# Kernel optimization log

Measured on AMD Instinct MI355X. Metric: run time of the kernel, lower is better.

The kernel has to match this reference:

```python
import jax, jax.numpy as jnp
import numpy as np

B, S, E, H, L, V = 4, 1024, 256, 512, 16, 8000


def setup_inputs() -> dict:
    key = jax.random.key(0)
    ks = jax.random.split(key, 8)
    return {
        "sent": jax.random.randint(ks[0], (B, S), 0, V),
        "mask": jax.random.randint(ks[1], (B, S), 0, 2),
        "char_emb_w": jax.random.normal(ks[2], (V, E), dtype=jnp.float32) * 0.02,
        "mask_emb_w": jax.random.normal(ks[3], (2, E), dtype=jnp.float32) * 0.02,
        "wA": jax.random.normal(ks[4], (E, H), dtype=jnp.float32) * (1.0 / np.sqrt(E)),
        "bA": jnp.zeros((H,), dtype=jnp.float32),
        "wB": jax.random.normal(ks[5], (E, H), dtype=jnp.float32) * (1.0 / np.sqrt(E)),
        "bB": jnp.zeros((H,), dtype=jnp.float32),
        "wS": jax.random.normal(ks[6], (E, L), dtype=jnp.float32) * (1.0 / np.sqrt(E)),
        "bS": jnp.zeros((L,), dtype=jnp.float32),
    }


def reference(sent, mask, char_emb_w, mask_emb_w, wA, bA, wB, bB, wS, bS):
    # Embedding lookups: (B,S,E)
    ce = char_emb_w[sent]
    me = mask_emb_w[mask]
    # vemb = char_emb * GELU(mask_emb)  (torch GELU default = exact erf form)
    vemb = ce * jax.nn.gelu(me, approximate=False)
    va = vemb @ wA + bA                      # (B,S,H)
    vb = jax.nn.sigmoid(vemb @ wB + bB)      # (B,S,H)
    vc = jnp.einsum("bih,bjh->bij", va, vb) / H   # (B,S,S), biaffine score
    vd = jax.nn.relu(vemb @ wS + bS)         # (B,S,L)
    # torch: matmul(vc.unsqueeze(3), vd.unsqueeze(2)) -> (B,S,S,L) rank-1 outer product
    pred = jax.nn.softmax(vc[..., None] * vd[:, :, None, :], axis=-1)
    return pred
```

## Files before the change

### kernel.cpp

```cpp
#include <hip/hip_runtime.h>
#include <hip/hip_bf16.h>
#include <math.h>

typedef __attribute__((ext_vector_type(8))) short short8;
typedef __attribute__((ext_vector_type(4))) float f32x4;
typedef unsigned short u16;

#define Bn 4
#define Sn 1024
#define En 256
#define Hn 512
#define Ln 16

__device__ inline u16 bf16b(float x) {
    union { __hip_bfloat16 h; u16 u; } cvt;
    cvt.h = __float2bfloat16(x);
    return cvt.u;
}

__global__ void prep_wt(const float* __restrict__ wA, const float* __restrict__ wB,
                        const float* __restrict__ wS, u16* __restrict__ Wt) {
    int idx = blockIdx.x * 256 + threadIdx.x;
    int n = idx >> 8;
    int k = idx & 255;
    float v = 0.f;
    if (n < 512)       v = wA[k * 512 + n];
    else if (n < 1024) v = wB[k * 512 + (n - 512)];
    else if (n < 1040) v = wS[k * 16 + (n - 1024)];
    Wt[idx] = bf16b(v);
}

__global__ void embed_gelu(const int* __restrict__ sent, const int* __restrict__ mask,
                           const float* __restrict__ ce_w, const float* __restrict__ me_w,
                           u16* __restrict__ vemb) {
    int row = blockIdx.x;
    int e = threadIdx.x;
    int s = sent[row];
    int m = mask[row];
    float ce = ce_w[s * En + e];
    float me = me_w[m * En + e];
    float g = 0.5f * me * (1.f + erff(me * 0.70710678118654752f));
    vemb[row * En + e] = bf16b(ce * g);
}

#define LDP 136
__global__ __launch_bounds__(256, 2) void gemm1(const u16* __restrict__ A, const u16* __restrict__ Bt,
                                                const float* __restrict__ bA, const float* __restrict__ bB,
                                                const float* __restrict__ bS,
                                                u16* __restrict__ va, u16* __restrict__ vb,
                                                float* __restrict__ vd) {
    __shared__ __align__(16) u16 As[64 * LDP];
    __shared__ __align__(16) u16 Bs[64 * LDP];
    int tid = threadIdx.x;
    int m0 = blockIdx.x * 64, n0 = blockIdx.y * 64;
    int lane = tid & 63, w = tid >> 6;
    int lrow = lane & 15, quad = lane >> 4;

    f32x4 acc[4];
    for (int nt = 0; nt < 4; nt++) acc[nt] = (f32x4){0.f, 0.f, 0.f, 0.f};

    for (int kb = 0; kb < 2; kb++) {
        for (int i = 0; i < 4; i++) {
            int off = (i * 256 + tid) * 8;
            int r = off >> 7, c = off & 127;
            *(short8*)&As[r * LDP + c] = *(const short8*)&A[(m0 + r) * 256 + kb * 128 + c];
            *(short8*)&Bs[r * LDP + c] = *(const short8*)&Bt[(n0 + r) * 256 + kb * 128 + c];
        }
        __syncthreads();
        for (int ks = 0; ks < 4; ks++) {
            short8 a = *(const short8*)&As[(w * 16 + lrow) * LDP + ks * 32 + quad * 8];
            for (int nt = 0; nt < 4; nt++) {
                short8 b = *(const short8*)&Bs[(nt * 16 + lrow) * LDP + ks * 32 + quad * 8];
                acc[nt] = __builtin_amdgcn_mfma_f32_16x16x32_bf16(a, b, acc[nt], 0, 0, 0);
            }
        }
        __syncthreads();
    }
    int mbase = m0 + w * 16 + quad * 4;
    for (int nt = 0; nt < 4; nt++) {
        int n = n0 + nt * 16 + lrow;
        for (int r = 0; r < 4; r++) {
            float v = acc[nt][r];
            int mm = mbase + r;
            if (n < 512) {
                va[mm * 512 + n] = bf16b(v + bA[n]);
            } else if (n < 1024) {
                float x = v + bB[n - 512];
                vb[mm * 512 + (n - 512)] = bf16b(1.f / (1.f + __expf(-x)));
            } else if (n < 1040) {
                float x = v + bS[n - 1024];
                vd[mm * 16 + (n - 1024)] = x > 0.f ? x : 0.f;
            }
        }
    }
}

__global__ void dminmax(const float* __restrict__ vd, float* __restrict__ dmn, float* __restrict__ dmx) {
    int r = blockIdx.x * 256 + threadIdx.x;
    float mn = 1e30f, mx = -1e30f;
    for (int l = 0; l < 16; l++) {
        float v = vd[r * 16 + l];
        mn = fminf(mn, v);
        mx = fmaxf(mx, v);
    }
    dmn[r] = mn;
    dmx[r] = mx;
}

__global__ __launch_bounds__(256, 2) void gemm2(const u16* __restrict__ va_g, const u16* __restrict__ vb_g,
                                                float* __restrict__ vc) {
    __shared__ __align__(16) u16 As[64 * LDP];
    __shared__ __align__(16) u16 Bs[64 * LDP];
    int tid = threadIdx.x;
    int b = blockIdx.z;
    int m0 = blockIdx.x * 64, n0 = blockIdx.y * 64;
    const u16* A  = va_g + (size_t)b * 1024 * 512;
    const u16* Bt = vb_g + (size_t)b * 1024 * 512;
    int lane = tid & 63, w = tid >> 6;
    int lrow = lane & 15, quad = lane >> 4;

    f32x4 acc[4];
    for (int nt = 0; nt < 4; nt++) acc[nt] = (f32x4){0.f, 0.f, 0.f, 0.f};

    for (int kb = 0; kb < 4; kb++) {
        for (int i = 0; i < 4; i++) {
            int off = (i * 256 + tid) * 8;
            int r = off >> 7, c = off & 127;
            *(short8*)&As[r * LDP + c] = *(const short8*)&A[(m0 + r) * 512 + kb * 128 + c];
            *(short8*)&Bs[r * LDP + c] = *(const short8*)&Bt[(n0 + r) * 512 + kb * 128 + c];
        }
        __syncthreads();
        for (int ks = 0; ks < 4; ks++) {
            short8 a = *(const short8*)&As[(w * 16 + lrow) * LDP + ks * 32 + quad * 8];
            for (int nt = 0; nt < 4; nt++) {
                short8 bfr = *(const short8*)&Bs[(nt * 16 + lrow) * LDP + ks * 32 + quad * 8];
                acc[nt] = __builtin_amdgcn_mfma_f32_16x16x32_bf16(a, bfr, acc[nt], 0, 0, 0);
            }
        }
        __syncthreads();
    }
    const float invH = 1.0f / 512.0f;
    float* C = vc + (size_t)b * 1024 * 1024;
    int mbase = m0 + w * 16 + quad * 4;
    for (int nt = 0; nt < 4; nt++) {
        int n = n0 + nt * 16 + lrow;
        for (int r = 0; r < 4; r++)
            C[(mbase + r) * 1024 + n] = acc[nt][r] * invH;
    }
}

__global__ __launch_bounds__(256) void expand(const float* __restrict__ vc, const float* __restrict__ vd,
                                              const float* __restrict__ dmn, const float* __restrict__ dmx,
                                              float* __restrict__ out) {
    int gid = blockIdx.x * 256 + threadIdx.x;
    int t = gid & 3;
    int grp = gid >> 2;
    int j = grp & 1023;
    int bi = grp >> 10;
    int b = bi >> 10;
    float c = vc[grp];
    int rowd = b * 1024 + j;
    float4 d = *(const float4*)&vd[rowd * 16 + t * 4];
    float m = (c >= 0.f) ? c * dmx[rowd] : c * dmn[rowd];
    float e0 = __expf(c * d.x - m);
    float e1 = __expf(c * d.y - m);
    float e2 = __expf(c * d.z - m);
    float e3 = __expf(c * d.w - m);
    float s = e0 + e1 + e2 + e3;
    s += __shfl_xor(s, 1);
    s += __shfl_xor(s, 2);
    float inv = 1.f / s;
    float4 o;
    o.x = e0 * inv; o.y = e1 * inv; o.z = e2 * inv; o.w = e3 * inv;
    *(float4*)&out[(size_t)grp * 16 + t * 4] = o;
}

extern "C" void kernel_launch(void* const* d_in, const int* in_sizes, int n_in,
                              void* d_out, int out_size, void* d_ws, size_t ws_size,
                              hipStream_t stream) {
    const int*   sent = (const int*)d_in[0];
    const int*   mask = (const int*)d_in[1];
    const float* ce_w = (const float*)d_in[2];
    const float* me_w = (const float*)d_in[3];
    const float* wA   = (const float*)d_in[4];
    const float* bA   = (const float*)d_in[5];
    const float* wB   = (const float*)d_in[6];
    const float* bB   = (const float*)d_in[7];
    const float* wS   = (const float*)d_in[8];
    const float* bS   = (const float*)d_in[9];
    float* out = (float*)d_out;

    char* ws = (char*)d_ws;
    u16* vemb = (u16*)ws;  ws += (size_t)4096 * 256 * 2;
    u16* Wt   = (u16*)ws;  ws += (size_t)1088 * 256 * 2;
    u16* va   = (u16*)ws;  ws += (size_t)4096 * 512 * 2;
    u16* vb   = (u16*)ws;  ws += (size_t)4096 * 512 * 2;
    float* vd  = (float*)ws;  ws += (size_t)4096 * 16 * 4;
    float* dmn = (float*)ws;  ws += (size_t)4096 * 4;
    float* dmx = (float*)ws;  ws += (size_t)4096 * 4;
    float* vc  = (float*)ws;  ws += (size_t)4 * 1024 * 1024 * 4;

    prep_wt<<<1088, 256, 0, stream>>>(wA, wB, wS, Wt);
    embed_gelu<<<4096, 256, 0, stream>>>(sent, mask, ce_w, me_w, vemb);
    gemm1<<<dim3(64, 17), 256, 0, stream>>>(vemb, Wt, bA, bB, bS, va, vb, vd);
    dminmax<<<16, 256, 0, stream>>>(vd, dmn, dmx);
    gemm2<<<dim3(16, 16, 4), 256, 0, stream>>>(va, vb, vc);
    expand<<<65536, 256, 0, stream>>>(vc, vd, dmn, dmx, out);
}
```

Measured before the change: 322.2 us.

## Fuse softmax expansion into biaffine GEMM epilogue and merge prep kernels

Moves the rank-1 outer-product softmax into the gemm2 epilogue, so the 16 MB fp32 vc intermediate is never written to or read back from global memory. It also folds the per-row min/max of vd into gemm1's epilogue using a shuffle reduction, and merges the weight-transpose and embedding kernels into one launch. This cuts three kernel launches and a large round-trip through memory. The cost is a heavier epilogue with 16 exps per element held in registers, and stores that are strided across the j dimension per lane, which may coalesce worse than the old expand kernel.

```diff
diff --git a/kernel.cpp b/kernel.cpp
--- a/kernel.cpp
+++ b/kernel.cpp
@@ -6,7 +6,6 @@
 typedef __attribute__((ext_vector_type(4))) float f32x4;
 typedef unsigned short u16;
 
-#define Bn 4
 #define Sn 1024
 #define En 256
 #define Hn 512
@@ -18,29 +17,31 @@
     return cvt.u;
 }
 
-__global__ void prep_wt(const float* __restrict__ wA, const float* __restrict__ wB,
-                        const float* __restrict__ wS, u16* __restrict__ Wt) {
-    int idx = blockIdx.x * 256 + threadIdx.x;
-    int n = idx >> 8;
-    int k = idx & 255;
-    float v = 0.f;
-    if (n < 512)       v = wA[k * 512 + n];
-    else if (n < 1024) v = wB[k * 512 + (n - 512)];
-    else if (n < 1040) v = wS[k * 16 + (n - 1024)];
-    Wt[idx] = bf16b(v);
-}
-
-__global__ void embed_gelu(const int* __restrict__ sent, const int* __restrict__ mask,
+__global__ void prep_embed(const float* __restrict__ wA, const float* __restrict__ wB,
+                           const float* __restrict__ wS, u16* __restrict__ Wt,
+                           const int* __restrict__ sent, const int* __restrict__ mask,
                            const float* __restrict__ ce_w, const float* __restrict__ me_w,
                            u16* __restrict__ vemb) {
-    int row = blockIdx.x;
-    int e = threadIdx.x;
-    int s = sent[row];
-    int m = mask[row];
-    float ce = ce_w[s * En + e];
-    float me = me_w[m * En + e];
-    float g = 0.5f * me * (1.f + erff(me * 0.70710678118654752f));
-    vemb[row * En + e] = bf16b(ce * g);
+    int bx = blockIdx.x;
+    if (bx < 1088) {
+        int idx = bx * 256 + threadIdx.x;
+        int n = idx >> 8;
+        int k = idx & 255;
+        float v = 0.f;
+        if (n < 512)       v = wA[k * 512 + n];
+        else if (n < 1024) v = wB[k * 512 + (n - 512)];
+        else if (n < 1040) v = wS[k * 16 + (n - 1024)];
+        Wt[idx] = bf16b(v);
+    } else {
+        int row = bx - 1088;
+        int e = threadIdx.x;
+        int s = sent[row];
+        int m = mask[row];
+        float ce = ce_w[s * En + e];
+        float me = me_w[m * En + e];
+        float g = 0.5f * me * (1.f + erff(me * 0.70710678118654752f));
+        vemb[row * En + e] = bf16b(ce * g);
+    }
 }
 
 #define LDP 136
@@ -48,7 +49,8 @@
                                                 const float* __restrict__ bA, const float* __restrict__ bB,
                                                 const float* __restrict__ bS,
                                                 u16* __restrict__ va, u16* __restrict__ vb,
-                                                float* __restrict__ vd) {
+                                                float* __restrict__ vd,
+                                                float* __restrict__ dmn, float* __restrict__ dmx) {
     __shared__ __align__(16) u16 As[64 * LDP];
     __shared__ __align__(16) u16 Bs[64 * LDP];
     int tid = threadIdx.x;
@@ -77,38 +79,47 @@
         __syncthreads();
     }
     int mbase = m0 + w * 16 + quad * 4;
-    for (int nt = 0; nt < 4; nt++) {
-        int n = n0 + nt * 16 + lrow;
+    if (blockIdx.y < 8) {
+        for (int nt = 0; nt < 4; nt++) {
+            int n = n0 + nt * 16 + lrow;
+            float bias = bA[n];
+            for (int r = 0; r < 4; r++)
+                va[(mbase + r) * 512 + n] = bf16b(acc[nt][r] + bias);
+        }
+    } else if (blockIdx.y < 16) {
+        for (int nt = 0; nt < 4; nt++) {
+            int n = n0 + nt * 16 + lrow - 512;
+            float bias = bB[n];
+            for (int r = 0; r < 4; r++) {
+                float x = acc[nt][r] + bias;
+                vb[(mbase + r) * 512 + n] = bf16b(1.f / (1.f + __expf(-x)));
+            }
+        }
+    } else {
+        float bias = bS[lrow];
         for (int r = 0; r < 4; r++) {
-            float v = acc[nt][r];
-            int mm = mbase + r;
-            if (n < 512) {
-                va[mm * 512 + n] = bf16b(v + bA[n]);
-            } else if (n < 1024) {
-                float x = v + bB[n - 512];
-                vb[mm * 512 + (n - 512)] = bf16b(1.f / (1.f + __expf(-x)));
-            } else if (n < 1040) {
-                float x = v + bS[n - 1024];
-                vd[mm * 16 + (n - 1024)] = x > 0.f ? x : 0.f;
-            }
-        }
-    }
-}
-
-__global__ void dminmax(const float* __restrict__ vd, float* __restrict__ dmn, float* __restrict__ dmx) {
-    int r = blockIdx.x * 256 + threadIdx.x;
-    float mn = 1e30f, mx = -1e30f;
-    for (int l = 0; l < 16; l++) {
-        float v = vd[r * 16 + l];
-        mn = fminf(mn, v);
-        mx = fmaxf(mx, v);
-    }
-    dmn[r] = mn;
-    dmx[r] = mx;
-}
-
-__global__ __launch_bounds__(256, 2) void gemm2(const u16* __restrict__ va_g, const u16* __restrict__ vb_g,
-                                                float* __restrict__ vc) {
+            float x = acc[0][r] + bias;
+            x = x > 0.f ? x : 0.f;
+            vd[(mbase + r) * 16 + lrow] = x;
+            float mn = x, mx = x;
+            for (int d = 1; d < 16; d <<= 1) {
+                mn = fminf(mn, __shfl_xor(mn, d));
+                mx = fmaxf(mx, __shfl_xor(mx, d));
+            }
+            if (lrow == 0) {
+                dmn[mbase + r] = mn;
+                dmx[mbase + r] = mx;
+            }
+        }
+    }
+}
+
+__global__ __launch_bounds__(256, 2) void gemm2_softmax(const u16* __restrict__ va_g,
+                                                        const u16* __restrict__ vb_g,
+                                                        const float* __restrict__ vd,
+                                                        const float* __restrict__ dmn,
+                                                        const float* __restrict__ dmx,
+                                                        float* __restrict__ out) {
     __shared__ __align__(16) u16 As[64 * LDP];
     __shared__ __align__(16) u16 Bs[64 * LDP];
     int tid = threadIdx.x;
@@ -139,40 +150,44 @@
         }
         __syncthreads();
     }
+
     const float invH = 1.0f / 512.0f;
-    float* C = vc + (size_t)b * 1024 * 1024;
     int mbase = m0 + w * 16 + quad * 4;
     for (int nt = 0; nt < 4; nt++) {
         int n = n0 + nt * 16 + lrow;
-        for (int r = 0; r < 4; r++)
-            C[(mbase + r) * 1024 + n] = acc[nt][r] * invH;
-    }
-}
-
-__global__ __launch_bounds__(256) void expand(const float* __restrict__ vc, const float* __restrict__ vd,
-                                              const float* __restrict__ dmn, const float* __restrict__ dmx,
-                                              float* __restrict__ out) {
-    int gid = blockIdx.x * 256 + threadIdx.x;
-    int t = gid & 3;
-    int grp = gid >> 2;
-    int j = grp & 1023;
-    int bi = grp >> 10;
-    int b = bi >> 10;
-    float c = vc[grp];
-    int rowd = b * 1024 + j;
-    float4 d = *(const float4*)&vd[rowd * 16 + t * 4];
-    float m = (c >= 0.f) ? c * dmx[rowd] : c * dmn[rowd];
-    float e0 = __expf(c * d.x - m);
-    float e1 = __expf(c * d.y - m);
-    float e2 = __expf(c * d.z - m);
-    float e3 = __expf(c * d.w - m);
-    float s = e0 + e1 + e2 + e3;
-    s += __shfl_xor(s, 1);
-    s += __shfl_xor(s, 2);
-    float inv = 1.f / s;
-    float4 o;
-    o.x = e0 * inv; o.y = e1 * inv; o.z = e2 * inv; o.w = e3 * inv;
-    *(float4*)&out[(size_t)grp * 16 + t * 4] = o;
+        int rowd = b * 1024 + n;
+        float4 d0 = *(const float4*)&vd[rowd * 16 + 0];
+        float4 d1 = *(const float4*)&vd[rowd * 16 + 4];
+        float4 d2 = *(const float4*)&vd[rowd * 16 + 8];
+        float4 d3 = *(const float4*)&vd[rowd * 16 + 12];
+        float mn = dmn[rowd], mx = dmx[rowd];
+        for (int r = 0; r < 4; r++) {
+            float c = acc[nt][r] * invH;
+            float m = (c >= 0.f) ? c * mx : c * mn;
+            float e[16];
+            e[0]  = __expf(c * d0.x - m); e[1]  = __expf(c * d0.y - m);
+            e[2]  = __expf(c * d0.z - m); e[3]  = __expf(c * d0.w - m);
+            e[4]  = __expf(c * d1.x - m); e[5]  = __expf(c * d1.y - m);
+            e[6]  = __expf(c * d1.z - m); e[7]  = __expf(c * d1.w - m);
+            e[8]  = __expf(c * d2.x - m); e[9]  = __expf(c * d2.y - m);
+            e[10] = __expf(c * d2.z - m); e[11] = __expf(c * d2.w - m);
+            e[12] = __expf(c * d3.x - m); e[13] = __expf(c * d3.y - m);
+            e[14] = __expf(c * d3.z - m); e[15] = __expf(c * d3.w - m);
+            float s = 0.f;
+            for (int l = 0; l < 16; l++) s += e[l];
+            float inv = 1.f / s;
+            size_t base = (((size_t)(b * 1024 + mbase + r)) * 1024 + n) * 16;
+            float4 o;
+            o.x = e[0] * inv;  o.y = e[1] * inv;  o.z = e[2] * inv;  o.w = e[3] * inv;
+            *(float4*)&out[base + 0] = o;
+            o.x = e[4] * inv;  o.y = e[5] * inv;  o.z = e[6] * inv;  o.w = e[7] * inv;
+            *(float4*)&out[base + 4] = o;
+            o.x = e[8] * inv;  o.y = e[9] * inv;  o.z = e[10] * inv; o.w = e[11] * inv;
+            *(float4*)&out[base + 8] = o;
+            o.x = e[12] * inv; o.y = e[13] * inv; o.z = e[14] * inv; o.w = e[15] * inv;
+            *(float4*)&out[base + 12] = o;
+        }
+    }
 }
 
 extern "C" void kernel_launch(void* const* d_in, const int* in_sizes, int n_in,
@@ -198,12 +213,8 @@
     float* vd  = (float*)ws;  ws += (size_t)4096 * 16 * 4;
     float* dmn = (float*)ws;  ws += (size_t)4096 * 4;
     float* dmx = (float*)ws;  ws += (size_t)4096 * 4;
-    float* vc  = (float*)ws;  ws += (size_t)4 * 1024 * 1024 * 4;
-
-    prep_wt<<<1088, 256, 0, stream>>>(wA, wB, wS, Wt);
-    embed_gelu<<<4096, 256, 0, stream>>>(sent, mask, ce_w, me_w, vemb);
-    gemm1<<<dim3(64, 17), 256, 0, stream>>>(vemb, Wt, bA, bB, bS, va, vb, vd);
-    dminmax<<<16, 256, 0, stream>>>(vd, dmn, dmx);
-    gemm2<<<dim3(16, 16, 4), 256, 0, stream>>>(va, vb, vc);
-    expand<<<65536, 256, 0, stream>>>(vc, vd, dmn, dmx, out);
-}
+
+    prep_embed<<<5184, 256, 0, stream>>>(wA, wB, wS, Wt, sent, mask, ce_w, me_w, vemb);
+    gemm1<<<dim3(64, 17), 256, 0, stream>>>(vemb, Wt, bA, bB, bS, va, vb, vd, dmn, dmx);
+    gemm2_softmax<<<dim3(16, 16, 4), 256, 0, stream>>>(va, vb, vd, dmn, dmx, out);
+}
```

Result: slower. 353.6 us (+9.8%).
